# Kernel optimization log

Hardware: AMD Instinct MI355X
Metric: run time of the kernel (lower is better)

The kernel has to match this reference:

```python
import jax, jax.numpy as jnp
import numpy as np

N_NODES = 16384
N_EDGES = 196608
N_ELEM = 8
C = 32              # hidden channels per l-block
LMAX = 3
SH_DIM = 16         # (LMAX+1)^2
NUM_BESSEL = 8
R_MAX = 5.0
P_CUT = 5.0
H_RAD = 64
AVG_NEIGH = 12.0
N_LAYERS = 2
L_SLICES = ((0, 1), (1, 4), (4, 9), (9, 16))  # l = 0..3 blocks


def real_sph_harm(u):
    # u: [E,3] unit vectors -> real spherical harmonics up to l=3, component-normalized. [E,16]
    x, y, z = u[:, 0], u[:, 1], u[:, 2]
    x2, y2, z2 = x * x, y * y, z * z
    sh = [
        jnp.ones_like(x),
        jnp.sqrt(3.) * x, jnp.sqrt(3.) * y, jnp.sqrt(3.) * z,
        jnp.sqrt(15.) * x * y, jnp.sqrt(15.) * y * z,
        jnp.sqrt(5.) / 2. * (3. * z2 - 1.), jnp.sqrt(15.) * x * z,
        jnp.sqrt(15.) / 2. * (x2 - y2),
        jnp.sqrt(35. / 8.) * y * (3. * x2 - y2), jnp.sqrt(105.) * x * y * z,
        jnp.sqrt(21. / 8.) * y * (5. * z2 - 1.), jnp.sqrt(7.) / 2. * z * (5. * z2 - 3.),
        jnp.sqrt(21. / 8.) * x * (5. * z2 - 1.), jnp.sqrt(105.) / 2. * z * (x2 - y2),
        jnp.sqrt(35. / 8.) * x * (x2 - 3. * y2),
    ]
    return jnp.stack(sh, axis=-1)


def bessel_cutoff(r):
    # Bessel radial basis * polynomial cutoff (MACE radial embedding). r: [E] -> [E, NUM_BESSEL]
    u = r / R_MAX
    n = jnp.arange(1, NUM_BESSEL + 1, dtype=r.dtype)
    safe_r = jnp.maximum(r, 1e-9)
    rb = jnp.sqrt(2.0 / R_MAX) * jnp.sin(jnp.pi * n * u[:, None]) / safe_r[:, None]
    p = P_CUT
    fc = 1.0 - (p + 1.) * (p + 2.) / 2. * u ** p + p * (p + 2.) * u ** (p + 1.) - p * (p + 1.) / 2. * u ** (p + 2.)
    fc = fc * (u < 1.0).astype(r.dtype)
    return rb * fc[:, None]


def per_l_linear(a, W):
    # equivariant per-l channel mixing. a: [N,C,16], W: [4,C,C]
    outs = [jnp.einsum('nci,co->noi', a[:, :, s:e], W[l]) for l, (s, e) in enumerate(L_SLICES)]
    return jnp.concatenate(outs, axis=-1)


def mace_descriptors(atom_pos, node_attrs, shifts, edge_index,
                     W_embed, W1, W2, W3, W4, Wlin, Wskip, w2, w3, Wprod):
    snd, rcv = edge_index[0], edge_index[1]
    vec = atom_pos[rcv] - atom_pos[snd] + shifts            # [E,3]
    length = jnp.sqrt(jnp.sum(vec * vec, axis=-1) + 1e-18)  # [E]
    unit = vec / length[:, None]
    edge_attrs = real_sph_harm(unit)                        # [E,16]
    edge_feats = bessel_cutoff(length)                      # [E,8]

    node_scal = node_attrs @ W_embed                        # [N,C] node embedding (l=0)
    node_feats = jnp.zeros((atom_pos.shape[0], C, SH_DIM), dtype=atom_pos.dtype).at[:, :, 0].set(node_scal)

    descs = []
    for i in range(N_LAYERS):
        # radial MLP -> per-edge tensor-product weights
        h = jax.nn.silu(edge_feats @ W1[i])
        h = jax.nn.silu(h @ W2[i])
        h = jax.nn.silu(h @ W3[i])
        tpw = (h @ W4[i]).reshape(-1, C, SH_DIM)            # [E,C,16]
        # gather -> channelwise tensor product with edge spherical harmonics
        s = node_feats[:, :, 0][snd]                        # [E,C] invariant sender feats
        msg = tpw * edge_attrs[:, None, :] * s[:, :, None]  # [E,C,16]
        # scatter-add aggregation
        agg = jax.ops.segment_sum(msg.reshape(-1, C * SH_DIM), rcv,
                                  num_segments=N_NODES) / AVG_NEIGH
        a = per_l_linear(agg.reshape(-1, C, SH_DIM), Wlin[i])
        # element-dependent residual (skip tensor product with one-hot node attrs)
        sc = jnp.einsum('nz,ncm,zco->nom', node_attrs, node_feats, Wskip[i])
        # symmetric-contraction-style product block (correlation up to 3, invariants)
        inv = a[:, :, 0]
        p2 = jnp.sum(a * a, axis=-1)                        # power-spectrum invariant [N,C]
        b0 = inv + w2[i] * p2 + w3[i] * inv * p2
        b = a.at[:, :, 0].set(b0)
        node_feats = per_l_linear(b, Wprod[i]) + sc
        descs.append(node_feats[:, :, 0])                   # invariant slice
    return jnp.concatenate(descs, axis=-1)                  # [N, N_LAYERS*C]


def setup_inputs() -> dict:
    key = jax.random.key(0)
    ks = jax.random.split(key, 16)
    atom_pos = jax.random.normal(ks[0], (N_NODES, 3), dtype=jnp.float32) * 1.8
    elem = jax.random.randint(ks[1], (N_NODES,), 0, N_ELEM)
    node_attrs = jax.nn.one_hot(elem, N_ELEM, dtype=jnp.float32)
    shifts = jnp.zeros((N_EDGES, 3), dtype=jnp.float32)
    edge_index = jax.random.randint(ks[2], (2, N_EDGES), 0, N_NODES)
    f32 = jnp.float32
    W_embed = jax.random.normal(ks[3], (N_ELEM, C), f32) / np.sqrt(N_ELEM)
    W1 = jax.random.normal(ks[4], (N_LAYERS, NUM_BESSEL, H_RAD), f32) / np.sqrt(NUM_BESSEL)
    W2 = jax.random.normal(ks[5], (N_LAYERS, H_RAD, H_RAD), f32) / np.sqrt(H_RAD)
    W3 = jax.random.normal(ks[6], (N_LAYERS, H_RAD, H_RAD), f32) / np.sqrt(H_RAD)
    W4 = jax.random.normal(ks[7], (N_LAYERS, H_RAD, C * SH_DIM), f32) / np.sqrt(H_RAD)
    Wlin = jax.random.normal(ks[8], (N_LAYERS, 4, C, C), f32) / np.sqrt(C)
    Wskip = jax.random.normal(ks[9], (N_LAYERS, N_ELEM, C, C), f32) / np.sqrt(N_ELEM * C)
    w2 = jax.random.normal(ks[10], (N_LAYERS, C), f32) * 0.1
    w3 = jax.random.normal(ks[11], (N_LAYERS, C), f32) * 0.1
    Wprod = jax.random.normal(ks[12], (N_LAYERS, 4, C, C), f32) / np.sqrt(C)
    return {"atom_pos": atom_pos, "node_attrs": node_attrs, "shifts": shifts,
            "edge_index": edge_index, "W_embed": W_embed, "W1": W1, "W2": W2,
            "W3": W3, "W4": W4, "Wlin": Wlin, "Wskip": Wskip, "w2": w2,
            "w3": w3, "Wprod": Wprod}


def reference(atom_pos, node_attrs, shifts, edge_index, W_embed, W1, W2, W3, W4,
              Wlin, Wskip, w2, w3, Wprod):
    return mace_descriptors(atom_pos, node_attrs, shifts, edge_index,
                            W_embed, W1, W2, W3, W4, Wlin, Wskip, w2, w3, Wprod)
```

## Files before the change

kernel.cpp:

```cpp
#include <hip/hip_runtime.h>
#include <math.h>

#define N_NODES_C 16384
#define N_EDGES_C 196608
#define MAX_TILES 32768

typedef short bf16x8 __attribute__((ext_vector_type(8)));
typedef float f32x4 __attribute__((ext_vector_type(4)));
typedef float f32x8 __attribute__((ext_vector_type(8)));

__device__ __forceinline__ float silu_f(float x) {
  return x * __builtin_amdgcn_rcpf(1.0f + __expf(-x));
}

__global__ void k_count(const int* __restrict__ rcv, int* __restrict__ counts) {
  int e = blockIdx.x * 256 + threadIdx.x;
  atomicAdd(&counts[rcv[e]], 1);
}

__global__ __launch_bounds__(1024) void k_scan(const int* __restrict__ counts,
                                               int* __restrict__ row_start,
                                               int* __restrict__ cursor,
                                               int* __restrict__ tstart) {
  __shared__ int s1a[1024];
  __shared__ int s2a[1024];
  const int tid = threadIdx.x;
  int loc[16];
  int s1 = 0, s2 = 0;
#pragma unroll
  for (int i = 0; i < 16; ++i) {
    loc[i] = counts[tid * 16 + i];
    s1 += loc[i];
    s2 += (loc[i] + 15) >> 4;
  }
  s1a[tid] = s1;
  s2a[tid] = s2;
  __syncthreads();
  for (int off = 1; off < 1024; off <<= 1) {
    int t1 = (tid >= off) ? s1a[tid - off] : 0;
    int t2 = (tid >= off) ? s2a[tid - off] : 0;
    __syncthreads();
    s1a[tid] += t1;
    s2a[tid] += t2;
    __syncthreads();
  }
  int e1 = s1a[tid] - s1, e2 = s2a[tid] - s2;
#pragma unroll
  for (int i = 0; i < 16; ++i) {
    row_start[tid * 16 + i] = e1;
    cursor[tid * 16 + i] = e1;
    tstart[tid * 16 + i] = e2;
    e1 += loc[i];
    e2 += (loc[i] + 15) >> 4;
  }
  if (tid == 1023) {
    row_start[N_NODES_C] = e1;
    tstart[N_NODES_C] = e2;
  }
}

__global__ void k_fill(const int* __restrict__ rcv, int* __restrict__ cursor,
                       int* __restrict__ elist) {
  int e = blockIdx.x * 256 + threadIdx.x;
  int slot = atomicAdd(&cursor[rcv[e]], 1);
  elist[slot] = e;
}

__global__ void k_tiles(const int* __restrict__ row_start, const int* __restrict__ tstart,
                        int2* __restrict__ tdesc) {
  const int n = blockIdx.x * 256 + threadIdx.x;
  const int e0 = row_start[n], e1 = row_start[n + 1];
  const int cnt = e1 - e0;
  const int nt = (cnt + 15) >> 4;
  const int t0 = tstart[n];
  const unsigned mbit = (nt > 1) ? 0x80000000u : 0u;
  for (int j = 0; j < nt; ++j) {
    int len = cnt - 16 * j;
    if (len > 16) len = 16;
    tdesc[t0 + j] = make_int2((int)((unsigned)n | ((unsigned)len << 20) | mbit), e0 + 16 * j);
  }
}

__global__ void k_elem(const float* __restrict__ attrs, int* __restrict__ elem) {
  int n = blockIdx.x * 256 + threadIdx.x;
  const float* a = attrs + n * 8;
  int best = 0;
  float bv = a[0];
#pragma unroll
  for (int z = 1; z < 8; ++z) {
    if (a[z] > bv) { bv = a[z]; best = z; }
  }
  elem[n] = best;
}

__global__ void k_embed(const float* __restrict__ attrs, const float* __restrict__ Wemb,
                        float* __restrict__ scal0, float* __restrict__ nf) {
  int gid = blockIdx.x * 256 + threadIdx.x;
  int n = gid >> 5, c = gid & 31;
  float s = 0.f;
#pragma unroll
  for (int z = 0; z < 8; ++z) s = fmaf(attrs[n * 8 + z], Wemb[z * 32 + c], s);
  scal0[gid] = s;
  float* row = nf + (size_t)n * 512 + c * 16;
  *(float4*)&row[0] = make_float4(s, 0.f, 0.f, 0.f);
  *(float4*)&row[4] = make_float4(0.f, 0.f, 0.f, 0.f);
  *(float4*)&row[8] = make_float4(0.f, 0.f, 0.f, 0.f);
  *(float4*)&row[12] = make_float4(0.f, 0.f, 0.f, 0.f);
}

__global__ __launch_bounds__(256, 3) void k_radial(
    const float* __restrict__ pos, const float* __restrict__ shifts,
    const int* __restrict__ snd, const int* __restrict__ rcv,
    const int* __restrict__ elist, const float* __restrict__ scal,
    const float* __restrict__ W1g, const float* __restrict__ W2g,
    const float* __restrict__ W3g, unsigned short* __restrict__ h3,
    float* __restrict__ sedge, float* __restrict__ Yout, const int writeY) {
  __shared__ __align__(16) float efs[4][32][8];
  __shared__ __align__(16) float hbs[4][2][64];
  const int wid = threadIdx.x >> 6, lane = threadIdx.x & 63;
  float w1c[8], w2c[64], w3c[64];
#pragma unroll
  for (int k = 0; k < 8; ++k) w1c[k] = W1g[k * 64 + lane];
#pragma unroll
  for (int k = 0; k < 64; ++k) w2c[k] = W2g[k * 64 + lane];
#pragma unroll
  for (int k = 0; k < 64; ++k) w3c[k] = W3g[k * 64 + lane];

  const int base = (blockIdx.x * 4 + wid) * 32;

  if (lane < 32) {
    const int p = base + lane;
    const int e = elist[p];
    const int sn = snd[e], rc = rcv[e];
    const float vx = pos[rc * 3 + 0] - pos[sn * 3 + 0] + shifts[e * 3 + 0];
    const float vy = pos[rc * 3 + 1] - pos[sn * 3 + 1] + shifts[e * 3 + 1];
    const float vz = pos[rc * 3 + 2] - pos[sn * 3 + 2] + shifts[e * 3 + 2];
    const float len = __builtin_amdgcn_sqrtf(vx * vx + vy * vy + vz * vz + 1e-18f);
    const float u = len * 0.2f;
    float fc = 0.f;
    if (u < 1.0f) {
      const float u2 = u * u, u5 = u2 * u2 * u;
      fc = 1.0f - 21.0f * u5 + 35.0f * u5 * u - 15.0f * u5 * u2;
    }
    const float pref = 0.6324555320336759f * fc * __builtin_amdgcn_rcpf(fmaxf(len, 1e-9f));
    float efv[8];
#pragma unroll
    for (int k = 0; k < 8; ++k) {
      const float pin = 3.14159274f * (float)(k + 1);
      efv[k] = pref * __sinf(pin * u);
    }
    *(float4*)&efs[wid][lane][0] = make_float4(efv[0], efv[1], efv[2], efv[3]);
    *(float4*)&efs[wid][lane][4] = make_float4(efv[4], efv[5], efv[6], efv[7]);

    if (writeY) {
      const float il = __builtin_amdgcn_rcpf(len);
      const float x = vx * il, y = vy * il, z = vz * il;
      const float x2 = x * x, y2 = y * y, z2 = z * z;
      const float s3 = 1.7320508075688772f;
      const float s15 = 3.872983346207417f;
      const float s5h = 1.118033988749895f;
      const float s35_8 = 2.091650066335189f;
      const float s105 = 10.246950765959598f;
      const float s21_8 = 1.6201851746019651f;
      const float s7h = 1.3228756555322954f;
      const float s105h = 5.123475382979799f;
      float* yp = Yout + (size_t)p * 16;
      *(float4*)&yp[0] = make_float4(1.f, s3 * x, s3 * y, s3 * z);
      *(float4*)&yp[4] = make_float4(s15 * x * y, s15 * y * z, s5h * (3.f * z2 - 1.f), s15 * x * z);
      *(float4*)&yp[8] = make_float4(0.5f * s15 * (x2 - y2), s35_8 * y * (3.f * x2 - y2),
                                     s105 * x * y * z, s21_8 * y * (5.f * z2 - 1.f));
      *(float4*)&yp[12] = make_float4(s7h * z * (5.f * z2 - 3.f), s21_8 * x * (5.f * z2 - 1.f),
                                      s105h * z * (x2 - y2), s35_8 * x * (x2 - 3.f * y2));
    }
  }

  {
    const int p2 = base + (lane >> 1);
    const int e2 = elist[p2];
    const int sn2 = snd[e2];
    const int co = (lane & 1) * 16;
    const float* sp = scal + (size_t)sn2 * 32 + co;
    float* dp = sedge + (size_t)p2 * 32 + co;
    *(float4*)&dp[0] = *(const float4*)&sp[0];
    *(float4*)&dp[4] = *(const float4*)&sp[4];
    *(float4*)&dp[8] = *(const float4*)&sp[8];
    *(float4*)&dp[12] = *(const float4*)&sp[12];
  }

  for (int t = 0; t < 16; ++t) {
    const float4 eA0 = *(const float4*)&efs[wid][t][0];
    const float4 eA1 = *(const float4*)&efs[wid][t][4];
    const float4 eB0 = *(const float4*)&efs[wid][t + 16][0];
    const float4 eB1 = *(const float4*)&efs[wid][t + 16][4];
    float aA = eA0.x * w1c[0], aB = eB0.x * w1c[0];
    aA = fmaf(eA0.y, w1c[1], aA); aB = fmaf(eB0.y, w1c[1], aB);
    aA = fmaf(eA0.z, w1c[2], aA); aB = fmaf(eB0.z, w1c[2], aB);
    aA = fmaf(eA0.w, w1c[3], aA); aB = fmaf(eB0.w, w1c[3], aB);
    aA = fmaf(eA1.x, w1c[4], aA); aB = fmaf(eB1.x, w1c[4], aB);
    aA = fmaf(eA1.y, w1c[5], aA); aB = fmaf(eB1.y, w1c[5], aB);
    aA = fmaf(eA1.z, w1c[6], aA); aB = fmaf(eB1.z, w1c[6], aB);
    aA = fmaf(eA1.w, w1c[7], aA); aB = fmaf(eB1.w, w1c[7], aB);
    hbs[wid][0][lane] = silu_f(aA);
    hbs[wid][1][lane] = silu_f(aB);
    float pA0 = 0.f, pA1 = 0.f, pA2 = 0.f, pA3 = 0.f;
    float pB0 = 0.f, pB1 = 0.f, pB2 = 0.f, pB3 = 0.f;
#pragma unroll
    for (int k4 = 0; k4 < 16; ++k4) {
      const float4 hA = *(const float4*)&hbs[wid][0][k4 * 4];
      const float4 hB = *(const float4*)&hbs[wid][1][k4 * 4];
      pA0 = fmaf(hA.x, w2c[k4 * 4 + 0], pA0); pB0 = fmaf(hB.x, w2c[k4 * 4 + 0], pB0);
      pA1 = fmaf(hA.y, w2c[k4 * 4 + 1], pA1); pB1 = fmaf(hB.y, w2c[k4 * 4 + 1], pB1);
      pA2 = fmaf(hA.z, w2c[k4 * 4 + 2], pA2); pB2 = fmaf(hB.z, w2c[k4 * 4 + 2], pB2);
      pA3 = fmaf(hA.w, w2c[k4 * 4 + 3], pA3); pB3 = fmaf(hB.w, w2c[k4 * 4 + 3], pB3);
    }
    hbs[wid][0][lane] = silu_f((pA0 + pA1) + (pA2 + pA3));
    hbs[wid][1][lane] = silu_f((pB0 + pB1) + (pB2 + pB3));
    pA0 = pA1 = pA2 = pA3 = 0.f;
    pB0 = pB1 = pB2 = pB3 = 0.f;
#pragma unroll
    for (int k4 = 0; k4 < 16; ++k4) {
      const float4 hA = *(const float4*)&hbs[wid][0][k4 * 4];
      const float4 hB = *(const float4*)&hbs[wid][1][k4 * 4];
      pA0 = fmaf(hA.x, w3c[k4 * 4 + 0], pA0); pB0 = fmaf(hB.x, w3c[k4 * 4 + 0], pB0);
      pA1 = fmaf(hA.y, w3c[k4 * 4 + 1], pA1); pB1 = fmaf(hB.y, w3c[k4 * 4 + 1], pB1);
      pA2 = fmaf(hA.z, w3c[k4 * 4 + 2], pA2); pB2 = fmaf(hB.z, w3c[k4 * 4 + 2], pB2);
      pA3 = fmaf(hA.w, w3c[k4 * 4 + 3], pA3); pB3 = fmaf(hB.w, w3c[k4 * 4 + 3], pB3);
    }
    const float hvA = silu_f((pA0 + pA1) + (pA2 + pA3));
    const float hvB = silu_f((pB0 + pB1) + (pB2 + pB3));
    const unsigned hbA = __float_as_uint(hvA) & 0xFFFF0000u;
    const unsigned hbB = __float_as_uint(hvB) & 0xFFFF0000u;
    const float loA = hvA - __uint_as_float(hbA);
    const float loB = hvB - __uint_as_float(hbB);
    h3[(size_t)(base + t) * 128 + lane] = (unsigned short)(hbA >> 16);
    h3[(size_t)(base + t) * 128 + 64 + lane] = (unsigned short)(__float_as_uint(loA) >> 16);
    h3[(size_t)(base + 16 + t) * 128 + lane] = (unsigned short)(hbB >> 16);
    h3[(size_t)(base + 16 + t) * 128 + 64 + lane] = (unsigned short)(__float_as_uint(loB) >> 16);
  }
}

#define MLOAD(K, tix)                                                         \
  {                                                                           \
    const int tic = ((tix) < ntiles) ? (tix) : (ntiles - 1);                  \
    const int2 td = tdesc[tic];                                               \
    M[K] = (unsigned)td.x;                                                    \
    P[K] = td.y;                                                              \
  }

#define DLOAD(K2)                                                             \
  {                                                                           \
    const int p0 = P[K2];                                                     \
    const int lend = (int)((M[K2] >> 20) & 31u);                              \
    const unsigned short* hp = h3 + (size_t)(p0 + lm) * 128 + grp * 8;        \
    A[K2][0] = *(const bf16x8*)(hp);                                          \
    A[K2][1] = *(const bf16x8*)(hp + 32);                                     \
    A[K2][2] = *(const bf16x8*)(hp + 64);                                     \
    A[K2][3] = *(const bf16x8*)(hp + 96);                                     \
    _Pragma("unroll") for (int r = 0; r < 4; ++r) {                           \
      const int rr = grp * 4 + r;                                             \
      const int pr = p0 + rr;                                                 \
      const float yr = Yb[(size_t)pr * 16 + lm];                              \
      const float Yv = ((rr < lend) ? yr : 0.f) * inv12;                      \
      const float4 s4 = *(const float4*)&sedge[(size_t)pr * 32 + cg * 4];     \
      YS[K2][r][0] = Yv * s4.x;                                               \
      YS[K2][r][1] = Yv * s4.y;                                               \
      YS[K2][r][2] = Yv * s4.z;                                               \
      YS[K2][r][3] = Yv * s4.w;                                               \
    }                                                                         \
  }

#define STEP(K)                                                               \
  {                                                                           \
    const unsigned mcur = M[K];                                               \
    MLOAD(K, tb + 4);                                                         \
    DLOAD((K + 2) & 3);                                                       \
    const int node = (int)(mcur & 0x3FFFu);                                   \
    const bool multi = (mcur & 0x80000000u) != 0u;                            \
    float outv[4];                                                            \
    _Pragma("unroll") for (int t = 0; t < 4; ++t) {                           \
      f32x4 acc = {0.f, 0.f, 0.f, 0.f};                                       \
      acc = __builtin_amdgcn_mfma_f32_16x16x32_bf16(A[K][0], bhi[t][0], acc, 0, 0, 0); \
      acc = __builtin_amdgcn_mfma_f32_16x16x32_bf16(A[K][1], bhi[t][1], acc, 0, 0, 0); \
      acc = __builtin_amdgcn_mfma_f32_16x16x32_bf16(A[K][2], bhi[t][0], acc, 0, 0, 0); \
      acc = __builtin_amdgcn_mfma_f32_16x16x32_bf16(A[K][3], bhi[t][1], acc, 0, 0, 0); \
      acc = __builtin_amdgcn_mfma_f32_16x16x32_bf16(A[K][0], blo[t][0], acc, 0, 0, 0); \
      acc = __builtin_amdgcn_mfma_f32_16x16x32_bf16(A[K][1], blo[t][1], acc, 0, 0, 0); \
      float cp = acc[0] * YS[K][0][t];                                        \
      cp = fmaf(acc[1], YS[K][1][t], cp);                                     \
      cp = fmaf(acc[2], YS[K][2][t], cp);                                     \
      cp = fmaf(acc[3], YS[K][3][t], cp);                                     \
      cp += __shfl_xor(cp, 16);                                               \
      cp += __shfl_xor(cp, 32);                                               \
      outv[t] = cp;                                                           \
    }                                                                         \
    float sel = outv[0];                                                      \
    sel = (grp == 1) ? outv[1] : sel;                                         \
    sel = (grp == 2) ? outv[2] : sel;                                         \
    sel = (grp == 3) ? outv[3] : sel;                                         \
    if (tb < ntiles) {                                                        \
      float* ap = &agg[(size_t)node * 512 + cg * 64 + grp * 16 + lm];         \
      if (multi)                                                              \
        atomicAdd(ap, sel);                                                   \
      else                                                                    \
        *ap = sel;                                                            \
    }                                                                         \
    ++tb;                                                                     \
  }

__global__ __launch_bounds__(256, 2) void k_gather(
    const unsigned short* __restrict__ h3, const float* __restrict__ W4g,
    const float* __restrict__ Yb, const float* __restrict__ sedge,
    const int2* __restrict__ tdesc, const int* __restrict__ ntiles_ptr,
    float* __restrict__ agg) {
  const int bid = blockIdx.x;
  const int xcd = bid & 7, q = bid >> 3, half = q & 1;
  const int s = ((q >> 1) << 3) | xcd;
  const int w = threadIdx.x >> 6, lane = threadIdx.x & 63;
  const int grp = lane >> 4, lm = lane & 15;
  const int cg = half * 4 + w;
  const float inv12 = 1.0f / 12.0f;

  bf16x8 bhi[4][2], blo[4][2];
#pragma unroll
  for (int t = 0; t < 4; ++t) {
    const int col = cg * 64 + t * 16 + lm;
#pragma unroll
    for (int kk = 0; kk < 2; ++kk) {
#pragma unroll
      for (int j = 0; j < 8; ++j) {
        const float wv = W4g[(kk * 32 + grp * 8 + j) * 512 + col];
        const unsigned hb = __float_as_uint(wv) & 0xFFFF0000u;
        bhi[t][kk][j] = (short)(hb >> 16);
        blo[t][kk][j] = (short)(__float_as_uint(wv - __uint_as_float(hb)) >> 16);
      }
    }
  }

  const int ntiles = *ntiles_ptr;
  const int chunk4 = ((((ntiles + 511) >> 9) + 3) & ~3);
  int tb = s * chunk4;

  bf16x8 A[4][4];
  float YS[4][4][4];
  unsigned M[4];
  int P[4];

  MLOAD(0, tb + 0);
  MLOAD(1, tb + 1);
  MLOAD(2, tb + 2);
  MLOAD(3, tb + 3);
  DLOAD(0);
  DLOAD(1);

  for (int jj = 0; jj < chunk4; jj += 4) {
    STEP(0);
    STEP(1);
    STEP(2);
    STEP(3);
  }
}

__global__ __launch_bounds__(256) void k_node(
    const float* __restrict__ agg, float* __restrict__ nf,
    const float* __restrict__ Wlin, const float* __restrict__ Wprod,
    const float* __restrict__ Wskip, const float* __restrict__ w2v,
    const float* __restrict__ w3v, const int* __restrict__ elem,
    float* __restrict__ scal_out, float* __restrict__ dout, const int layer) {
  __shared__ __align__(16) float aggs[8][512];
  __shared__ __align__(16) float nfs[8][512];
  __shared__ float bs[8][544];
  const int tid = threadIdx.x;
  const int n0 = blockIdx.x * 8;
  for (int i = tid; i < 1024; i += 256) {
    const int nl = i >> 7, qq = i & 127;
    ((f32x4*)aggs)[i] = ((const f32x4*)agg)[(size_t)(n0 + nl) * 128 + qq];
    ((f32x4*)nfs)[i] = ((const f32x4*)nf)[(size_t)(n0 + nl) * 128 + qq];
  }
  __syncthreads();
  const int nl = tid >> 5, o = tid & 31;
  const int n = n0 + nl;
  constexpr int SLa[4] = {0, 1, 4, 9};
  constexpr int ELa[4] = {1, 4, 9, 16};
  float a[16];
#pragma unroll
  for (int m = 0; m < 16; ++m) a[m] = 0.f;
#pragma unroll
  for (int l = 0; l < 4; ++l) {
    for (int c = 0; c < 32; ++c) {
      const float w = Wlin[(l * 32 + c) * 32 + o];
#pragma unroll
      for (int m = SLa[l]; m < ELa[l]; ++m) a[m] = fmaf(aggs[nl][c * 16 + m], w, a[m]);
    }
  }
  const float inv = a[0];
  float p2 = 0.f;
#pragma unroll
  for (int m = 0; m < 16; ++m) p2 = fmaf(a[m], a[m], p2);
  a[0] = inv + w2v[o] * p2 + w3v[o] * inv * p2;
#pragma unroll
  for (int m = 0; m < 16; ++m) bs[nl][o * 17 + m] = a[m];
  __syncthreads();
  float outv[16];
#pragma unroll
  for (int m = 0; m < 16; ++m) outv[m] = 0.f;
#pragma unroll
  for (int l = 0; l < 4; ++l) {
    for (int c = 0; c < 32; ++c) {
      const float w = Wprod[(l * 32 + c) * 32 + o];
#pragma unroll
      for (int m = SLa[l]; m < ELa[l]; ++m) outv[m] = fmaf(bs[nl][c * 17 + m], w, outv[m]);
    }
  }
  const int z = elem[n];
  const float* wsk = Wskip + z * 1024;
  for (int c = 0; c < 32; ++c) {
    const float w = wsk[c * 32 + o];
#pragma unroll
    for (int m = 0; m < 16; ++m) outv[m] = fmaf(nfs[nl][c * 16 + m], w, outv[m]);
  }
  float* op = nf + (size_t)n * 512 + o * 16;
  *(float4*)&op[0] = make_float4(outv[0], outv[1], outv[2], outv[3]);
  *(float4*)&op[4] = make_float4(outv[4], outv[5], outv[6], outv[7]);
  *(float4*)&op[8] = make_float4(outv[8], outv[9], outv[10], outv[11]);
  *(float4*)&op[12] = make_float4(outv[12], outv[13], outv[14], outv[15]);
  scal_out[n * 32 + o] = outv[0];
  dout[(size_t)n * 64 + layer * 32 + o] = outv[0];
}

extern "C" void kernel_launch(void* const* d_in, const int* in_sizes, int n_in,
                              void* d_out, int out_size, void* d_ws, size_t ws_size,
                              hipStream_t stream) {
  const float* pos = (const float*)d_in[0];
  const float* attrs = (const float*)d_in[1];
  const float* shifts = (const float*)d_in[2];
  const int* eidx = (const int*)d_in[3];
  const float* W_embed = (const float*)d_in[4];
  const float* W1 = (const float*)d_in[5];
  const float* W2 = (const float*)d_in[6];
  const float* W3 = (const float*)d_in[7];
  const float* W4 = (const float*)d_in[8];
  const float* Wlin = (const float*)d_in[9];
  const float* Wskip = (const float*)d_in[10];
  const float* w2v = (const float*)d_in[11];
  const float* w3v = (const float*)d_in[12];
  const float* Wprod = (const float*)d_in[13];
  float* out = (float*)d_out;
  const int* snd = eidx;
  const int* rcv = eidx + N_EDGES_C;

  char* p = (char*)d_ws;
  auto take = [&](size_t bytes) {
    char* q = p;
    p += (bytes + 255) & ~(size_t)255;
    return q;
  };
  int* counts = (int*)take((size_t)N_NODES_C * 4);
  int* row_start = (int*)take((size_t)(N_NODES_C + 1) * 4);
  int* cursor = (int*)take((size_t)N_NODES_C * 4);
  int* tstart = (int*)take((size_t)(N_NODES_C + 1) * 4);
  int* elist = (int*)take((size_t)N_EDGES_C * 4);
  int2* tdesc = (int2*)take((size_t)MAX_TILES * 8);
  int* elem = (int*)take((size_t)N_NODES_C * 4);
  float* Ybuf = (float*)take((size_t)(N_EDGES_C + 16) * 16 * 4);
  unsigned short* h3 = (unsigned short*)take((size_t)(N_EDGES_C + 16) * 128 * 2);
  float* sedge = (float*)take((size_t)(N_EDGES_C + 16) * 32 * 4);
  float* agg = (float*)take((size_t)N_NODES_C * 512 * 4);
  float* nf = (float*)take((size_t)N_NODES_C * 512 * 4);
  float* scal0 = (float*)take((size_t)N_NODES_C * 32 * 4);
  float* scal1 = (float*)take((size_t)N_NODES_C * 32 * 4);
  (void)ws_size; (void)in_sizes; (void)n_in; (void)out_size;

  hipMemsetAsync(counts, 0, (size_t)N_NODES_C * 4, stream);
  k_count<<<N_EDGES_C / 256, 256, 0, stream>>>(rcv, counts);
  k_scan<<<1, 1024, 0, stream>>>(counts, row_start, cursor, tstart);
  k_fill<<<N_EDGES_C / 256, 256, 0, stream>>>(rcv, cursor, elist);
  k_tiles<<<N_NODES_C / 256, 256, 0, stream>>>(row_start, tstart, tdesc);
  k_elem<<<N_NODES_C / 256, 256, 0, stream>>>(attrs, elem);
  k_embed<<<N_NODES_C * 32 / 256, 256, 0, stream>>>(attrs, W_embed, scal0, nf);

  for (int i = 0; i < 2; ++i) {
    k_radial<<<1536, 256, 0, stream>>>(pos, shifts, snd, rcv, elist,
                                       i == 0 ? scal0 : scal1,
                                       W1 + (size_t)i * 8 * 64, W2 + (size_t)i * 64 * 64,
                                       W3 + (size_t)i * 64 * 64, h3, sedge, Ybuf,
                                       i == 0 ? 1 : 0);
    hipMemsetAsync(agg, 0, (size_t)N_NODES_C * 512 * 4, stream);
    k_gather<<<1024, 256, 0, stream>>>(h3, W4 + (size_t)i * 64 * 512, Ybuf, sedge,
                                       tdesc, tstart + N_NODES_C, agg);
    k_node<<<N_NODES_C / 8, 256, 0, stream>>>(agg, nf, Wlin + (size_t)i * 4096,
                                              Wprod + (size_t)i * 4096,
                                              Wskip + (size_t)i * 8192,
                                              w2v + (size_t)i * 32, w3v + (size_t)i * 32,
                                              elem, scal1, out, i);
  }
}
```

Baseline: 515.1 us.

## Run radial MLP on MFMA with split-bf16 hi/lo emulation of fp32

Replaces the scalar FMA radial MLP (8→64→64→64) with bf16 MFMA 16x16x32 instructions, using hi/lo bf16 splitting of weights and activations to keep near-fp32 accuracy. Weights are held in registers as MFMA B-fragments. Each wave now processes six 16-edge groups, with a padded LDS transpose between layers. The grid shrinks to 512 blocks and launch bounds drop to 2 waves per SIMD. Outputs are written as vectorized h3 rows. The cost is three MFMAs per product plus packing overhead and higher register pressure.

Result: faster. 446.5 us (-13.3%).

```diff
diff --git a/kernel.cpp b/kernel.cpp
--- a/kernel.cpp
+++ b/kernel.cpp
@@ -6,6 +6,7 @@
 #define MAX_TILES 32768
 
 typedef short bf16x8 __attribute__((ext_vector_type(8)));
+typedef unsigned short u16x8 __attribute__((ext_vector_type(8)));
 typedef float f32x4 __attribute__((ext_vector_type(4)));
 typedef float f32x8 __attribute__((ext_vector_type(8)));
 
@@ -108,28 +109,57 @@
   *(float4*)&row[12] = make_float4(0.f, 0.f, 0.f, 0.f);
 }
 
-__global__ __launch_bounds__(256, 3) void k_radial(
+__global__ __launch_bounds__(256, 2) void k_radial(
     const float* __restrict__ pos, const float* __restrict__ shifts,
     const int* __restrict__ snd, const int* __restrict__ rcv,
     const int* __restrict__ elist, const float* __restrict__ scal,
     const float* __restrict__ W1g, const float* __restrict__ W2g,
     const float* __restrict__ W3g, unsigned short* __restrict__ h3,
     float* __restrict__ sedge, float* __restrict__ Yout, const int writeY) {
-  __shared__ __align__(16) float efs[4][32][8];
-  __shared__ __align__(16) float hbs[4][2][64];
+  __shared__ unsigned tb[4][64 * 17];
   const int wid = threadIdx.x >> 6, lane = threadIdx.x & 63;
-  float w1c[8], w2c[64], w3c[64];
-#pragma unroll
-  for (int k = 0; k < 8; ++k) w1c[k] = W1g[k * 64 + lane];
-#pragma unroll
-  for (int k = 0; k < 64; ++k) w2c[k] = W2g[k * 64 + lane];
-#pragma unroll
-  for (int k = 0; k < 64; ++k) w3c[k] = W3g[k * 64 + lane];
-
-  const int base = (blockIdx.x * 4 + wid) * 32;
-
-  if (lane < 32) {
-    const int p = base + lane;
+  const int grp = lane >> 4, lm = lane & 15;
+  unsigned* tw = tb[wid];
+
+  bf16x8 b1hi[4], b1lo[4];
+#pragma unroll
+  for (int t = 0; t < 4; ++t) {
+#pragma unroll
+    for (int j = 0; j < 8; ++j) {
+      const float wv = (grp == 0) ? W1g[j * 64 + t * 16 + lm] : 0.f;
+      const unsigned hb = __float_as_uint(wv) & 0xFFFF0000u;
+      b1hi[t][j] = (short)(hb >> 16);
+      b1lo[t][j] = (short)(__float_as_uint(wv - __uint_as_float(hb)) >> 16);
+    }
+  }
+  bf16x8 b2hi[4][2], b2lo[4][2], b3hi[4][2], b3lo[4][2];
+#pragma unroll
+  for (int t = 0; t < 4; ++t) {
+#pragma unroll
+    for (int kf = 0; kf < 2; ++kf) {
+#pragma unroll
+      for (int j = 0; j < 8; ++j) {
+        const int widx = (kf * 32 + grp * 8 + j) * 64 + t * 16 + lm;
+        {
+          const float wv = W2g[widx];
+          const unsigned hb = __float_as_uint(wv) & 0xFFFF0000u;
+          b2hi[t][kf][j] = (short)(hb >> 16);
+          b2lo[t][kf][j] = (short)(__float_as_uint(wv - __uint_as_float(hb)) >> 16);
+        }
+        {
+          const float wv = W3g[widx];
+          const unsigned hb = __float_as_uint(wv) & 0xFFFF0000u;
+          b3hi[t][kf][j] = (short)(hb >> 16);
+          b3lo[t][kf][j] = (short)(__float_as_uint(wv - __uint_as_float(hb)) >> 16);
+        }
+      }
+    }
+  }
+
+  const int wv_id = blockIdx.x * 4 + wid;
+  for (int g = 0; g < 6; ++g) {
+    const int p0 = (wv_id * 6 + g) * 16;
+    const int p = p0 + lm;
     const int e = elist[p];
     const int sn = snd[e], rc = rcv[e];
     const float vx = pos[rc * 3 + 0] - pos[sn * 3 + 0] + shifts[e * 3 + 0];
@@ -143,14 +173,12 @@
       fc = 1.0f - 21.0f * u5 + 35.0f * u5 * u - 15.0f * u5 * u2;
     }
     const float pref = 0.6324555320336759f * fc * __builtin_amdgcn_rcpf(fmaxf(len, 1e-9f));
-    float efv[8];
+    float ef[8];
 #pragma unroll
     for (int k = 0; k < 8; ++k) {
       const float pin = 3.14159274f * (float)(k + 1);
-      efv[k] = pref * __sinf(pin * u);
-    }
-    *(float4*)&efs[wid][lane][0] = make_float4(efv[0], efv[1], efv[2], efv[3]);
-    *(float4*)&efs[wid][lane][4] = make_float4(efv[4], efv[5], efv[6], efv[7]);
+      ef[k] = pref * __sinf(pin * u);
+    }
 
     if (writeY) {
       const float il = __builtin_amdgcn_rcpf(len);
@@ -164,78 +192,129 @@
       const float s21_8 = 1.6201851746019651f;
       const float s7h = 1.3228756555322954f;
       const float s105h = 5.123475382979799f;
-      float* yp = Yout + (size_t)p * 16;
-      *(float4*)&yp[0] = make_float4(1.f, s3 * x, s3 * y, s3 * z);
-      *(float4*)&yp[4] = make_float4(s15 * x * y, s15 * y * z, s5h * (3.f * z2 - 1.f), s15 * x * z);
-      *(float4*)&yp[8] = make_float4(0.5f * s15 * (x2 - y2), s35_8 * y * (3.f * x2 - y2),
-                                     s105 * x * y * z, s21_8 * y * (5.f * z2 - 1.f));
-      *(float4*)&yp[12] = make_float4(s7h * z * (5.f * z2 - 3.f), s21_8 * x * (5.f * z2 - 1.f),
-                                      s105h * z * (x2 - y2), s35_8 * x * (x2 - 3.f * y2));
-    }
-  }
-
-  {
-    const int p2 = base + (lane >> 1);
-    const int e2 = elist[p2];
-    const int sn2 = snd[e2];
-    const int co = (lane & 1) * 16;
-    const float* sp = scal + (size_t)sn2 * 32 + co;
-    float* dp = sedge + (size_t)p2 * 32 + co;
-    *(float4*)&dp[0] = *(const float4*)&sp[0];
-    *(float4*)&dp[4] = *(const float4*)&sp[4];
-    *(float4*)&dp[8] = *(const float4*)&sp[8];
-    *(float4*)&dp[12] = *(const float4*)&sp[12];
-  }
-
-  for (int t = 0; t < 16; ++t) {
-    const float4 eA0 = *(const float4*)&efs[wid][t][0];
-    const float4 eA1 = *(const float4*)&efs[wid][t][4];
-    const float4 eB0 = *(const float4*)&efs[wid][t + 16][0];
-    const float4 eB1 = *(const float4*)&efs[wid][t + 16][4];
-    float aA = eA0.x * w1c[0], aB = eB0.x * w1c[0];
-    aA = fmaf(eA0.y, w1c[1], aA); aB = fmaf(eB0.y, w1c[1], aB);
-    aA = fmaf(eA0.z, w1c[2], aA); aB = fmaf(eB0.z, w1c[2], aB);
-    aA = fmaf(eA0.w, w1c[3], aA); aB = fmaf(eB0.w, w1c[3], aB);
-    aA = fmaf(eA1.x, w1c[4], aA); aB = fmaf(eB1.x, w1c[4], aB);
-    aA = fmaf(eA1.y, w1c[5], aA); aB = fmaf(eB1.y, w1c[5], aB);
-    aA = fmaf(eA1.z, w1c[6], aA); aB = fmaf(eB1.z, w1c[6], aB);
-    aA = fmaf(eA1.w, w1c[7], aA); aB = fmaf(eB1.w, w1c[7], aB);
-    hbs[wid][0][lane] = silu_f(aA);
-    hbs[wid][1][lane] = silu_f(aB);
-    float pA0 = 0.f, pA1 = 0.f, pA2 = 0.f, pA3 = 0.f;
-    float pB0 = 0.f, pB1 = 0.f, pB2 = 0.f, pB3 = 0.f;
-#pragma unroll
-    for (int k4 = 0; k4 < 16; ++k4) {
-      const float4 hA = *(const float4*)&hbs[wid][0][k4 * 4];
-      const float4 hB = *(const float4*)&hbs[wid][1][k4 * 4];
-      pA0 = fmaf(hA.x, w2c[k4 * 4 + 0], pA0); pB0 = fmaf(hB.x, w2c[k4 * 4 + 0], pB0);
-      pA1 = fmaf(hA.y, w2c[k4 * 4 + 1], pA1); pB1 = fmaf(hB.y, w2c[k4 * 4 + 1], pB1);
-      pA2 = fmaf(hA.z, w2c[k4 * 4 + 2], pA2); pB2 = fmaf(hB.z, w2c[k4 * 4 + 2], pB2);
-      pA3 = fmaf(hA.w, w2c[k4 * 4 + 3], pA3); pB3 = fmaf(hB.w, w2c[k4 * 4 + 3], pB3);
-    }
-    hbs[wid][0][lane] = silu_f((pA0 + pA1) + (pA2 + pA3));
-    hbs[wid][1][lane] = silu_f((pB0 + pB1) + (pB2 + pB3));
-    pA0 = pA1 = pA2 = pA3 = 0.f;
-    pB0 = pB1 = pB2 = pB3 = 0.f;
-#pragma unroll
-    for (int k4 = 0; k4 < 16; ++k4) {
-      const float4 hA = *(const float4*)&hbs[wid][0][k4 * 4];
-      const float4 hB = *(const float4*)&hbs[wid][1][k4 * 4];
-      pA0 = fmaf(hA.x, w3c[k4 * 4 + 0], pA0); pB0 = fmaf(hB.x, w3c[k4 * 4 + 0], pB0);
-      pA1 = fmaf(hA.y, w3c[k4 * 4 + 1], pA1); pB1 = fmaf(hB.y, w3c[k4 * 4 + 1], pB1);
-      pA2 = fmaf(hA.z, w3c[k4 * 4 + 2], pA2); pB2 = fmaf(hB.z, w3c[k4 * 4 + 2], pB2);
-      pA3 = fmaf(hA.w, w3c[k4 * 4 + 3], pA3); pB3 = fmaf(hB.w, w3c[k4 * 4 + 3], pB3);
-    }
-    const float hvA = silu_f((pA0 + pA1) + (pA2 + pA3));
-    const float hvB = silu_f((pB0 + pB1) + (pB2 + pB3));
-    const unsigned hbA = __float_as_uint(hvA) & 0xFFFF0000u;
-    const unsigned hbB = __float_as_uint(hvB) & 0xFFFF0000u;
-    const float loA = hvA - __uint_as_float(hbA);
-    const float loB = hvB - __uint_as_float(hbB);
-    h3[(size_t)(base + t) * 128 + lane] = (unsigned short)(hbA >> 16);
-    h3[(size_t)(base + t) * 128 + 64 + lane] = (unsigned short)(__float_as_uint(loA) >> 16);
-    h3[(size_t)(base + 16 + t) * 128 + lane] = (unsigned short)(hbB >> 16);
-    h3[(size_t)(base + 16 + t) * 128 + 64 + lane] = (unsigned short)(__float_as_uint(loB) >> 16);
+      float4 yq = make_float4(1.f, s3 * x, s3 * y, s3 * z);
+      if (grp == 1)
+        yq = make_float4(s15 * x * y, s15 * y * z, s5h * (3.f * z2 - 1.f), s15 * x * z);
+      if (grp == 2)
+        yq = make_float4(0.5f * s15 * (x2 - y2), s35_8 * y * (3.f * x2 - y2),
+                         s105 * x * y * z, s21_8 * y * (5.f * z2 - 1.f));
+      if (grp == 3)
+        yq = make_float4(s7h * z * (5.f * z2 - 3.f), s21_8 * x * (5.f * z2 - 1.f),
+                         s105h * z * (x2 - y2), s35_8 * x * (x2 - 3.f * y2));
+      *(float4*)&Yout[(size_t)p * 16 + grp * 4] = yq;
+    }
+
+    {
+      const float4 sa = *(const float4*)&scal[(size_t)sn * 32 + grp * 8];
+      const float4 sb = *(const float4*)&scal[(size_t)sn * 32 + grp * 8 + 4];
+      *(float4*)&sedge[(size_t)p * 32 + grp * 8] = sa;
+      *(float4*)&sedge[(size_t)p * 32 + grp * 8 + 4] = sb;
+    }
+
+    bf16x8 a1hi, a1lo;
+#pragma unroll
+    for (int j = 0; j < 8; ++j) {
+      const float v = (grp == 0) ? ef[j] : 0.f;
+      const unsigned hb = __float_as_uint(v) & 0xFFFF0000u;
+      a1hi[j] = (short)(hb >> 16);
+      a1lo[j] = (short)(__float_as_uint(v - __uint_as_float(hb)) >> 16);
+    }
+    f32x4 acc[4];
+#pragma unroll
+    for (int t = 0; t < 4; ++t) {
+      f32x4 a = {0.f, 0.f, 0.f, 0.f};
+      a = __builtin_amdgcn_mfma_f32_16x16x32_bf16(a1hi, b1hi[t], a, 0, 0, 0);
+      a = __builtin_amdgcn_mfma_f32_16x16x32_bf16(a1lo, b1hi[t], a, 0, 0, 0);
+      a = __builtin_amdgcn_mfma_f32_16x16x32_bf16(a1hi, b1lo[t], a, 0, 0, 0);
+      acc[t] = a;
+    }
+#pragma unroll
+    for (int t = 0; t < 4; ++t)
+#pragma unroll
+      for (int r = 0; r < 4; ++r) {
+        const float v = silu_f(acc[t][r]);
+        const unsigned hb = __float_as_uint(v) & 0xFFFF0000u;
+        tw[(t * 16 + lm) * 17 + grp * 4 + r] =
+            hb | (__float_as_uint(v - __uint_as_float(hb)) >> 16);
+      }
+    bf16x8 a2h0, a2h1, a2l0, a2l1;
+#pragma unroll
+    for (int j = 0; j < 8; ++j) {
+      const unsigned u0 = tw[(grp * 8 + j) * 17 + lm];
+      const unsigned u1 = tw[(32 + grp * 8 + j) * 17 + lm];
+      a2h0[j] = (short)(u0 >> 16);
+      a2l0[j] = (short)(u0 & 0xFFFFu);
+      a2h1[j] = (short)(u1 >> 16);
+      a2l1[j] = (short)(u1 & 0xFFFFu);
+    }
+#pragma unroll
+    for (int t = 0; t < 4; ++t) {
+      f32x4 a = {0.f, 0.f, 0.f, 0.f};
+      a = __builtin_amdgcn_mfma_f32_16x16x32_bf16(a2h0, b2hi[t][0], a, 0, 0, 0);
+      a = __builtin_amdgcn_mfma_f32_16x16x32_bf16(a2h1, b2hi[t][1], a, 0, 0, 0);
+      a = __builtin_amdgcn_mfma_f32_16x16x32_bf16(a2l0, b2hi[t][0], a, 0, 0, 0);
+      a = __builtin_amdgcn_mfma_f32_16x16x32_bf16(a2l1, b2hi[t][1], a, 0, 0, 0);
+      a = __builtin_amdgcn_mfma_f32_16x16x32_bf16(a2h0, b2lo[t][0], a, 0, 0, 0);
+      a = __builtin_amdgcn_mfma_f32_16x16x32_bf16(a2h1, b2lo[t][1], a, 0, 0, 0);
+      acc[t] = a;
+    }
+#pragma unroll
+    for (int t = 0; t < 4; ++t)
+#pragma unroll
+      for (int r = 0; r < 4; ++r) {
+        const float v = silu_f(acc[t][r]);
+        const unsigned hb = __float_as_uint(v) & 0xFFFF0000u;
+        tw[(t * 16 + lm) * 17 + grp * 4 + r] =
+            hb | (__float_as_uint(v - __uint_as_float(hb)) >> 16);
+      }
+    bf16x8 a3h0, a3h1, a3l0, a3l1;
+#pragma unroll
+    for (int j = 0; j < 8; ++j) {
+      const unsigned u0 = tw[(grp * 8 + j) * 17 + lm];
+      const unsigned u1 = tw[(32 + grp * 8 + j) * 17 + lm];
+      a3h0[j] = (short)(u0 >> 16);
+      a3l0[j] = (short)(u0 & 0xFFFFu);
+      a3h1[j] = (short)(u1 >> 16);
+      a3l1[j] = (short)(u1 & 0xFFFFu);
+    }
+#pragma unroll
+    for (int t = 0; t < 4; ++t) {
+      f32x4 a = {0.f, 0.f, 0.f, 0.f};
+      a = __builtin_amdgcn_mfma_f32_16x16x32_bf16(a3h0, b3hi[t][0], a, 0, 0, 0);
+      a = __builtin_amdgcn_mfma_f32_16x16x32_bf16(a3h1, b3hi[t][1], a, 0, 0, 0);
+      a = __builtin_amdgcn_mfma_f32_16x16x32_bf16(a3l0, b3hi[t][0], a, 0, 0, 0);
+      a = __builtin_amdgcn_mfma_f32_16x16x32_bf16(a3l1, b3hi[t][1], a, 0, 0, 0);
+      a = __builtin_amdgcn_mfma_f32_16x16x32_bf16(a3h0, b3lo[t][0], a, 0, 0, 0);
+      a = __builtin_amdgcn_mfma_f32_16x16x32_bf16(a3h1, b3lo[t][1], a, 0, 0, 0);
+      acc[t] = a;
+    }
+#pragma unroll
+    for (int t = 0; t < 4; ++t)
+#pragma unroll
+      for (int r = 0; r < 4; ++r) {
+        const float v = silu_f(acc[t][r]);
+        const unsigned hb = __float_as_uint(v) & 0xFFFF0000u;
+        tw[(t * 16 + lm) * 17 + grp * 4 + r] =
+            hb | (__float_as_uint(v - __uint_as_float(hb)) >> 16);
+      }
+    {
+      const int eo = lane >> 2, q = lane & 3;
+      unsigned short* hrow = h3 + (size_t)(p0 + eo) * 128;
+      u16x8 h0, h1, l0v, l1v;
+#pragma unroll
+      for (int j = 0; j < 8; ++j) {
+        const unsigned ua = tw[(q * 16 + j) * 17 + eo];
+        const unsigned ub = tw[(q * 16 + 8 + j) * 17 + eo];
+        h0[j] = (unsigned short)(ua >> 16);
+        l0v[j] = (unsigned short)(ua & 0xFFFFu);
+        h1[j] = (unsigned short)(ub >> 16);
+        l1v[j] = (unsigned short)(ub & 0xFFFFu);
+      }
+      *(u16x8*)(hrow + q * 16) = h0;
+      *(u16x8*)(hrow + q * 16 + 8) = h1;
+      *(u16x8*)(hrow + 64 + q * 16) = l0v;
+      *(u16x8*)(hrow + 64 + q * 16 + 8) = l1v;
+    }
   }
 }
 
@@ -479,11 +558,11 @@
   k_embed<<<N_NODES_C * 32 / 256, 256, 0, stream>>>(attrs, W_embed, scal0, nf);
 
   for (int i = 0; i < 2; ++i) {
-    k_radial<<<1536, 256, 0, stream>>>(pos, shifts, snd, rcv, elist,
-                                       i == 0 ? scal0 : scal1,
-                                       W1 + (size_t)i * 8 * 64, W2 + (size_t)i * 64 * 64,
-                                       W3 + (size_t)i * 64 * 64, h3, sedge, Ybuf,
-                                       i == 0 ? 1 : 0);
+    k_radial<<<512, 256, 0, stream>>>(pos, shifts, snd, rcv, elist,
+                                      i == 0 ? scal0 : scal1,
+                                      W1 + (size_t)i * 8 * 64, W2 + (size_t)i * 64 * 64,
+                                      W3 + (size_t)i * 64 * 64, h3, sedge, Ybuf,
+                                      i == 0 ? 1 : 0);
     hipMemsetAsync(agg, 0, (size_t)N_NODES_C * 512 * 4, stream);
     k_gather<<<1024, 256, 0, stream>>>(h3, W4 + (size_t)i * 64 * 512, Ybuf, sedge,
                                        tdesc, tstart + N_NODES_C, agg);
```
